# Performance work log

Hardware: AMD Instinct MI355X
Metric: run time of the kernel (lower is better)

The kernel has to match this reference:

```python
import jax, jax.numpy as jnp
import numpy as np

N = 4096
CIN = 128
COUT = 128
J = 2
SLOPE = 0.2        # LeakyReLU negative slope (GAT-style)
NEG = -9.0e15      # mask fill value from the source
ATT = J * COUT     # att_slice


def _leaky(v):
    return jnp.where(v >= 0, v, SLOPE * v)


def setup_inputs() -> dict:
    key = jax.random.key(0)
    ks = jax.random.split(key, 12)
    x = jax.random.normal(ks[0], (N, CIN), dtype=jnp.float32)

    def sparse_op(k):
        kv, km = jax.random.split(k)
        vals = jax.random.normal(kv, (N, N), dtype=jnp.float32)
        mask = jax.random.uniform(km, (N, N)) < 0.05
        return jnp.where(mask, vals, 0.0)

    Lu = sparse_op(ks[1])
    Ld = sparse_op(ks[2])
    P = jax.random.normal(ks[3], (N, N), dtype=jnp.float32) * 0.01  # harmonic projector

    s = 1.0 / np.sqrt(CIN)
    Wi_w = jax.random.uniform(ks[4], (J, CIN, COUT), minval=-s, maxval=s)
    Wi_b = jax.random.uniform(ks[5], (J, COUT), minval=-s, maxval=s)
    Ws_w = jax.random.uniform(ks[6], (J, CIN, COUT), minval=-s, maxval=s)
    Ws_b = jax.random.uniform(ks[7], (J, COUT), minval=-s, maxval=s)
    Wh_w = jax.random.uniform(ks[8], (CIN, COUT), minval=-s, maxval=s)
    Wh_b = jax.random.uniform(ks[9], (COUT,), minval=-s, maxval=s)
    att_irr = jax.random.normal(ks[10], (2 * ATT, 1), dtype=jnp.float32) * 0.1
    att_sol = jax.random.normal(ks[11], (2 * ATT, 1), dtype=jnp.float32) * 0.1
    return {"x": x, "Lu": Lu, "Ld": Ld, "P": P,
            "Wi_w": Wi_w, "Wi_b": Wi_b, "Ws_w": Ws_w, "Ws_b": Ws_b,
            "Wh_w": Wh_w, "Wh_b": Wh_b, "att_irr": att_irr, "att_sol": att_sol}


def reference(x, Lu, Ld, P, Wi_w, Wi_b, Ws_w, Ws_b, Wh_w, Wh_b, att_irr, att_sol):
    n = x.shape[0]
    # concat_j W_irr[j](x) -> [N, J*COUT] (j-major matches torch.cat along dim=1)
    x_irr = (jnp.einsum('nc,jco->njo', x, Wi_w) + Wi_b[None]).reshape(n, ATT)
    x_sol = (jnp.einsum('nc,jco->njo', x, Ws_w) + Ws_b[None]).reshape(n, ATT)

    # GAT-style scores: E[i,j] = leaky(s1[i] + s2[j])
    E_irr = _leaky(x_irr @ att_irr[:ATT] + (x_irr @ att_irr[ATT:]).T)
    E_sol = _leaky(x_sol @ att_sol[:ATT] + (x_sol @ att_sol[ATT:]).T)
    E_irr = jnp.where(Ld != 0, E_irr, NEG)
    E_sol = jnp.where(Lu != 0, E_sol, NEG)
    alpha_irr = jax.nn.softmax(E_irr, axis=1)  # dropout: eval mode -> identity
    alpha_sol = jax.nn.softmax(E_sol, axis=1)

    z = (alpha_irr @ x) @ Wi_w[0] + Wi_b[0] + (alpha_sol @ x) @ Ws_w[0] + Ws_b[0]
    for p in range(1, J):  # Laplacian-power aggregation
        alpha_irr = alpha_irr @ Ld
        alpha_sol = alpha_sol @ Lu
        z = z + (alpha_irr @ x) @ Wi_w[p] + Wi_b[p]
        z = z + (alpha_sol @ x) @ Ws_w[p] + Ws_b[p]
    z = z + (P @ x) @ Wh_w + Wh_b
    return z
```

## Files before the change

kernel.cpp:

```cpp
#include <hip/hip_runtime.h>

#define NN 4096
#define IDX_CAP 512
#define SEG_CAP 160
#define SLOPE 0.2f

typedef float f4_t __attribute__((ext_vector_type(4)));
typedef __bf16 bf8v __attribute__((ext_vector_type(8)));
typedef float f32x16 __attribute__((ext_vector_type(16)));

#define V_OFF     0
#define C_OFF     512
#define BT_OFF    516
#define S_OFF     1024
#define HXI_OFF   32768
#define HXS_OFF   (HXI_OFF + NN*128)
#define UI_OFF    (HXS_OFF + NN*128)
#define US_OFF    (UI_OFF + NN*128)
#define XWH_OFF   (US_OFF + NN*128)
#define OI_OFF    (XWH_OFF + NN*128)
#define OS_OFF    (OI_OFF + NN*128)
#define ZP_OFF    (OS_OFF + NN*128)
#define WS_FLOATS (ZP_OFF + 8*NN*128)
#define IDX_BYTE_OFF ((size_t)WS_FLOATS * 4)
#define CNT_BYTE_OFF (IDX_BYTE_OFF + (size_t)2*NN*IDX_CAP*2)

#define XI(c)   ((c) + (((c) >> 5) << 2))

#define MAP_BR(bid)   (((bid) >> 2) & 1)
#define MAP_ROW(bid)  ((((bid) >> 3) << 2) | ((bid) & 3))

__device__ __forceinline__ unsigned short f2bf(float x) {
  unsigned u = __float_as_uint(x);
  return (unsigned short)((u + 0x7FFFu + ((u >> 16) & 1u)) >> 16);
}
__device__ __forceinline__ float bf2f(unsigned short h) {
  return __uint_as_float(((unsigned)h) << 16);
}
union BFU { unsigned short u[8]; bf8v v; };

__global__ __launch_bounds__(128) void k_prep(
    const float* __restrict__ Wi_w, const float* __restrict__ Wi_b,
    const float* __restrict__ Ws_w, const float* __restrict__ Ws_b,
    const float* __restrict__ Wh_b, const float* __restrict__ att_irr,
    const float* __restrict__ att_sol, float* __restrict__ ws) {
  const int t = threadIdx.x;
  float v1i = 0.f, v2i = 0.f, v1s = 0.f, v2s = 0.f;
  for (int j = 0; j < 2; ++j) {
    for (int o = 0; o < 128; ++o) {
      const float wi = Wi_w[j*16384 + t*128 + o];
      const float wv = Ws_w[j*16384 + t*128 + o];
      v1i += wi * att_irr[j*128 + o];
      v2i += wi * att_irr[256 + j*128 + o];
      v1s += wv * att_sol[j*128 + o];
      v2s += wv * att_sol[256 + j*128 + o];
    }
  }
  ws[V_OFF + t]       = v1i;
  ws[V_OFF + 128 + t] = v2i;
  ws[V_OFF + 256 + t] = v1s;
  ws[V_OFF + 384 + t] = v2s;
  ws[BT_OFF + t] = Wi_b[t] + Wi_b[128 + t] + Ws_b[t] + Ws_b[128 + t] + Wh_b[t];
  if (t < 4) {
    const float* bb = (t < 2) ? Wi_b : Ws_b;
    const float* aa = ((t < 2) ? att_irr : att_sol) + ((t & 1) ? 256 : 0);
    float c = 0.f;
    for (int k = 0; k < 256; ++k) c += bb[k] * aa[k];
    ws[C_OFF + t] = c;
  }
}

__global__ __launch_bounds__(256) void k_pre2(
    const float* __restrict__ x, const float* __restrict__ Wh_w,
    float* __restrict__ ws, unsigned short* __restrict__ xth,
    unsigned short* __restrict__ xtl) {
  __shared__ __align__(16) float At[32][33];
  __shared__ __align__(16) float Wt[32][144];
  const int t = threadIdx.x;

  if (blockIdx.x < 128) {
    const int rb = blockIdx.x;
    const int rg = t >> 4, cg = t & 15;
    const int r0 = rb * 32;
    float acc[2][8];
    #pragma unroll
    for (int i = 0; i < 2; ++i)
      #pragma unroll
      for (int j = 0; j < 8; ++j) acc[i][j] = 0.f;
    for (int k0 = 0; k0 < 128; k0 += 32) {
      __syncthreads();
      {
        const int row = t >> 3, kq = t & 7;
        const float4 av = *(const float4*)&x[(r0 + row)*128 + k0 + kq*4];
        At[row][kq*4+0] = av.x; At[row][kq*4+1] = av.y;
        At[row][kq*4+2] = av.z; At[row][kq*4+3] = av.w;
      }
      #pragma unroll
      for (int l = 0; l < 4; ++l) {
        const int idx = t + l*256;
        const int kr = idx >> 5, c4 = idx & 31;
        const float4 wv = *(const float4*)&Wh_w[(k0 + kr)*128 + c4*4];
        *(float4*)&Wt[kr][XI(c4*4)] = wv;
      }
      __syncthreads();
      #pragma unroll
      for (int k = 0; k < 32; ++k) {
        const float a0 = At[rg*2 + 0][k];
        const float a1 = At[rg*2 + 1][k];
        const float4 b0 = *(const float4*)&Wt[k][XI(cg*8)];
        const float4 b1 = *(const float4*)&Wt[k][XI(cg*8 + 4)];
        acc[0][0] += a0*b0.x; acc[0][1] += a0*b0.y; acc[0][2] += a0*b0.z; acc[0][3] += a0*b0.w;
        acc[0][4] += a0*b1.x; acc[0][5] += a0*b1.y; acc[0][6] += a0*b1.z; acc[0][7] += a0*b1.w;
        acc[1][0] += a1*b0.x; acc[1][1] += a1*b0.y; acc[1][2] += a1*b0.z; acc[1][3] += a1*b0.w;
        acc[1][4] += a1*b1.x; acc[1][5] += a1*b1.y; acc[1][6] += a1*b1.z; acc[1][7] += a1*b1.w;
      }
    }
    #pragma unroll
    for (int i = 0; i < 2; ++i) {
      const int r = r0 + rg*2 + i;
      #pragma unroll
      for (int j = 0; j < 8; ++j) {
        const int c = cg*8 + j;
        const float val = acc[i][j];
        const unsigned short h = f2bf(val);
        const unsigned short l = f2bf(val - bf2f(h));
        xth[(size_t)c*NN + r] = h;
        xtl[(size_t)c*NN + r] = l;
      }
    }
  } else {
    const int wave = t >> 6, lane = t & 63;
    const int row = (blockIdx.x - 128) * 4 + wave;
    const float* v = ws + V_OFF;
    const float x0 = x[row*128 + lane];
    const float x1 = x[row*128 + 64 + lane];
    float p0 = x0 * v[lane]       + x1 * v[64 + lane];
    float p1 = x0 * v[128 + lane] + x1 * v[192 + lane];
    float p2 = x0 * v[256 + lane] + x1 * v[320 + lane];
    float p3 = x0 * v[384 + lane] + x1 * v[448 + lane];
    #pragma unroll
    for (int off = 32; off; off >>= 1) {
      p0 += __shfl_down(p0, off);
      p1 += __shfl_down(p1, off);
      p2 += __shfl_down(p2, off);
      p3 += __shfl_down(p3, off);
    }
    if (lane == 0) {
      ws[S_OFF + row]          = p0 + ws[C_OFF + 0];
      ws[S_OFF + NN + row]     = p1 + ws[C_OFF + 1];
      ws[S_OFF + 2*NN + row]   = p2 + ws[C_OFF + 2];
      ws[S_OFF + 3*NN + row]   = p3 + ws[C_OFF + 3];
    }
  }
}

__global__ __launch_bounds__(256) void k_spmm_emit(
    const float* __restrict__ Ld, const float* __restrict__ Lu,
    const float* __restrict__ x, float* __restrict__ ws,
    unsigned short* __restrict__ idxbuf, int* __restrict__ cntbuf) {
  const int bid = blockIdx.x;
  const int br  = MAP_BR(bid);
  const int row = MAP_ROW(bid);
  const float* __restrict__ Lrow = (br ? Lu : Ld) + (size_t)row * NN;
  float* __restrict__ Hx = ws + (br ? HXS_OFF : HXI_OFF);
  unsigned short* __restrict__ idxg = idxbuf + (size_t)(br*NN + row) * IDX_CAP;
  const int t = threadIdx.x;
  const int w = t >> 6, lane = t & 63;
  const unsigned long long lmask = (1ull << lane) - 1ull;

  __shared__ short jseg[4][SEG_CAP];
  __shared__ float vseg[4][SEG_CAP];
  __shared__ int   wcnt[4];
  __shared__ int   off[5];
  __shared__ short jl[IDX_CAP];
  __shared__ float vl[IDX_CAP];
  __shared__ float red[4][128];

  const f4_t* __restrict__ Lrow4 = (const f4_t*)Lrow;
  f4_t lv[4];
  #pragma unroll
  for (int i = 0; i < 4; ++i) lv[i] = __builtin_nontemporal_load(&Lrow4[i*256 + t]);

  int base = 0;
  #pragma unroll
  for (int i = 0; i < 4; ++i) {
    #pragma unroll
    for (int c = 0; c < 4; ++c) {
      const float v = lv[i][c];
      const unsigned long long bm = __ballot(v != 0.f);
      if (v != 0.f) {
        const int pos = base + (int)__popcll(bm & lmask);
        if (pos < SEG_CAP) {
          jseg[w][pos] = (short)((i*256 + t)*4 + c);
          vseg[w][pos] = v;
        }
      }
      base += (int)__popcll(bm);
    }
  }
  if (lane == 0) wcnt[w] = base;
  __syncthreads();
  if (t == 0) {
    int o = 0, ov = 0;
    #pragma unroll
    for (int s = 0; s < 4; ++s) { off[s] = o; ov |= (wcnt[s] > SEG_CAP); o += wcnt[s]; }
    off[4] = (ov || o > IDX_CAP) ? (IDX_CAP + 1) : o;
    cntbuf[br*NN + row] = off[4];
  }
  __syncthreads();
  const int m = off[4];

  if (m <= IDX_CAP) {
    const int o = off[w], c = wcnt[w];
    for (int k = lane; k < c; k += 64) {
      const short j = jseg[w][k];
      jl[o + k] = j;
      vl[o + k] = vseg[w][k];
      idxg[o + k] = (unsigned short)j;
    }
  }
  __syncthreads();

  if (m <= IDX_CAP) {
    const f4_t* __restrict__ x4 = (const f4_t*)x;
    const int li = lane & 31, half = lane >> 5;
    f4_t acc = {0.f, 0.f, 0.f, 0.f};
    int p = w;
    for (; 2*(p + 12) + 1 < m; p += 16) {
      const int q0 = 2*p + half, q1 = 2*(p+4) + half,
                q2 = 2*(p+8) + half, q3 = 2*(p+12) + half;
      const int j0 = jl[q0], j1 = jl[q1], j2 = jl[q2], j3 = jl[q3];
      const float v0 = vl[q0], v1 = vl[q1], v2 = vl[q2], v3 = vl[q3];
      const f4_t g0 = x4[j0*32 + li];
      const f4_t g1 = x4[j1*32 + li];
      const f4_t g2 = x4[j2*32 + li];
      const f4_t g3 = x4[j3*32 + li];
      acc += v0*g0; acc += v1*g1; acc += v2*g2; acc += v3*g3;
    }
    for (; 2*p < m; p += 4) {
      const int q = 2*p + half;
      if (q < m) acc += vl[q] * x4[jl[q]*32 + li];
    }
    #pragma unroll
    for (int c = 0; c < 4; ++c) acc[c] += __shfl_xor(acc[c], 32);
    if (half == 0) {
      red[w][li*4+0] = acc[0]; red[w][li*4+1] = acc[1];
      red[w][li*4+2] = acc[2]; red[w][li*4+3] = acc[3];
    }
  } else {
    const float2* __restrict__ x2 = (const float2*)x;
    float acc0 = 0.f, acc1 = 0.f;
    for (int j = w*1024; j < (w+1)*1024; ++j) {
      const float v = Lrow[j];
      if (v != 0.f) {
        const float2 g = x2[j*64 + lane];
        acc0 += v*g.x; acc1 += v*g.y;
      }
    }
    red[w][lane*2]     = acc0;
    red[w][lane*2 + 1] = acc1;
  }
  __syncthreads();
  if (t < 128)
    Hx[row*128 + t] = red[0][t] + red[1][t] + red[2][t] + red[3][t];
}

__global__ __launch_bounds__(256) void k_ugemm(
    const float* __restrict__ x, const float* __restrict__ Wi_w,
    const float* __restrict__ Ws_w, float* __restrict__ ws) {
  const int rb = blockIdx.x;
  const int sel = blockIdx.y;
  const float* A[2]; const float* W[2]; float* out;
  if (sel == 0) { A[0]=x; W[0]=Wi_w; A[1]=ws+HXI_OFF; W[1]=Wi_w+16384; out=ws+UI_OFF; }
  else          { A[0]=x; W[0]=Ws_w; A[1]=ws+HXS_OFF; W[1]=Ws_w+16384; out=ws+US_OFF; }

  __shared__ __align__(16) float At[32][33];
  __shared__ __align__(16) float Wt[32][144];
  const int t = threadIdx.x;
  const int rg = t >> 4, cg = t & 15;
  const int r0 = rb * 32;
  float acc[2][8];
  #pragma unroll
  for (int i = 0; i < 2; ++i)
    #pragma unroll
    for (int j = 0; j < 8; ++j) acc[i][j] = 0.f;

  for (int ps = 0; ps < 2; ++ps) {
    const float* __restrict__ Ap = A[ps];
    const float* __restrict__ Wp = W[ps];
    for (int k0 = 0; k0 < 128; k0 += 32) {
      __syncthreads();
      {
        const int row = t >> 3, kq = t & 7;
        const float4 av = *(const float4*)&Ap[(r0 + row)*128 + k0 + kq*4];
        At[row][kq*4+0] = av.x; At[row][kq*4+1] = av.y;
        At[row][kq*4+2] = av.z; At[row][kq*4+3] = av.w;
      }
      #pragma unroll
      for (int l = 0; l < 4; ++l) {
        const int idx = t + l*256;
        const int kr = idx >> 5, c4 = idx & 31;
        const float4 wv = *(const float4*)&Wp[(k0 + kr)*128 + c4*4];
        *(float4*)&Wt[kr][XI(c4*4)] = wv;
      }
      __syncthreads();
      #pragma unroll
      for (int k = 0; k < 32; ++k) {
        const float a0 = At[rg*2 + 0][k];
        const float a1 = At[rg*2 + 1][k];
        const float4 b0 = *(const float4*)&Wt[k][XI(cg*8)];
        const float4 b1 = *(const float4*)&Wt[k][XI(cg*8 + 4)];
        acc[0][0] += a0*b0.x; acc[0][1] += a0*b0.y; acc[0][2] += a0*b0.z; acc[0][3] += a0*b0.w;
        acc[0][4] += a0*b1.x; acc[0][5] += a0*b1.y; acc[0][6] += a0*b1.z; acc[0][7] += a0*b1.w;
        acc[1][0] += a1*b0.x; acc[1][1] += a1*b0.y; acc[1][2] += a1*b0.z; acc[1][3] += a1*b0.w;
        acc[1][4] += a1*b1.x; acc[1][5] += a1*b1.y; acc[1][6] += a1*b1.z; acc[1][7] += a1*b1.w;
      }
    }
  }
  #pragma unroll
  for (int i = 0; i < 2; ++i) {
    const int r = r0 + rg*2 + i;
    #pragma unroll
    for (int j = 0; j < 8; ++j) out[r*128 + cg*8 + j] = acc[i][j];
  }
}

__global__ __launch_bounds__(256) void k_attn(
    const float* __restrict__ Ld, const float* __restrict__ Lu,
    float* __restrict__ ws, const unsigned short* __restrict__ idxbuf,
    const int* __restrict__ cntbuf) {
  const int bid = blockIdx.x;
  const int br  = MAP_BR(bid);
  const int row = MAP_ROW(bid);
  const float* __restrict__ U = ws + (br ? US_OFF : UI_OFF);
  float* __restrict__ O = ws + (br ? OS_OFF : OI_OFF);
  const float s1 = ws[S_OFF + (br ? 2*NN : 0) + row];
  const float* __restrict__ s2a = ws + S_OFF + (br ? 3*NN : NN);
  const int cnt = cntbuf[br*NN + row];
  const int t = threadIdx.x;
  const int w = t >> 6, lane = t & 63;

  __shared__ int   jl[IDX_CAP];
  __shared__ float el[IDX_CAP];
  __shared__ float red[4][128];
  __shared__ float rsum[256];
  __shared__ float dsh[4];

  if (cnt > 0 && cnt <= IDX_CAP) {
    const unsigned short* __restrict__ idx = idxbuf + (size_t)(br*NN + row) * IDX_CAP;
    float dpart = 0.f;
    for (int p = t; p < cnt; p += 256) {
      const int j = idx[p];
      const float sc = s1 + s2a[j];
      const float e = expf(sc >= 0.f ? sc : SLOPE * sc);
      jl[p] = j; el[p] = e; dpart += e;
    }
    rsum[t] = dpart;
    __syncthreads();
    if (t < 128) rsum[t] += rsum[t + 128];
    __syncthreads();
    if (t < 64) {
      float v = rsum[t] + rsum[t + 64];
      #pragma unroll
      for (int off = 32; off; off >>= 1) v += __shfl_down(v, off);
      if (t == 0) dsh[0] = v;
    }
    __syncthreads();
    const float den = dsh[0];
    const f4_t* __restrict__ U4 = (const f4_t*)U;
    const int li = lane & 31, half = lane >> 5;
    f4_t acc = {0.f, 0.f, 0.f, 0.f};
    int p = w;
    for (; 2*(p + 12) + 1 < cnt; p += 16) {
      const int q0 = 2*p + half, q1 = 2*(p+4) + half,
                q2 = 2*(p+8) + half, q3 = 2*(p+12) + half;
      const int j0 = jl[q0], j1 = jl[q1], j2 = jl[q2], j3 = jl[q3];
      const float e0 = el[q0], e1 = el[q1], e2 = el[q2], e3 = el[q3];
      const f4_t g0 = U4[j0*32 + li];
      const f4_t g1 = U4[j1*32 + li];
      const f4_t g2 = U4[j2*32 + li];
      const f4_t g3 = U4[j3*32 + li];
      acc += e0*g0; acc += e1*g1; acc += e2*g2; acc += e3*g3;
    }
    for (; 2*p < cnt; p += 4) {
      const int q = 2*p + half;
      if (q < cnt) acc += el[q] * U4[jl[q]*32 + li];
    }
    #pragma unroll
    for (int c = 0; c < 4; ++c) acc[c] += __shfl_xor(acc[c], 32);
    if (half == 0) {
      red[w][li*4+0] = acc[0]; red[w][li*4+1] = acc[1];
      red[w][li*4+2] = acc[2]; red[w][li*4+3] = acc[3];
    }
    __syncthreads();
    if (t < 128)
      O[row*128 + t] = (red[0][t] + red[1][t] + red[2][t] + red[3][t]) / den;
  } else if (cnt == 0) {
    const float2* __restrict__ U2 = (const float2*)U;
    float acc0 = 0.f, acc1 = 0.f;
    for (int j = w*1024; j < (w+1)*1024; ++j) {
      const float2 g = U2[j*64 + lane];
      acc0 += g.x; acc1 += g.y;
    }
    red[w][lane*2]     = acc0;
    red[w][lane*2 + 1] = acc1;
    __syncthreads();
    if (t < 128)
      O[row*128 + t] = (red[0][t] + red[1][t] + red[2][t] + red[3][t]) * (1.f / NN);
  } else {
    const float* __restrict__ Lrow = (br ? Lu : Ld) + (size_t)row * NN;
    const float2* __restrict__ U2 = (const float2*)U;
    float acc0 = 0.f, acc1 = 0.f, dp = 0.f;
    for (int j = w*1024; j < (w+1)*1024; ++j) {
      const float v = Lrow[j];
      if (v != 0.f) {
        const float sc = s1 + s2a[j];
        const float e = expf(sc >= 0.f ? sc : SLOPE * sc);
        const float2 g = U2[j*64 + lane];
        acc0 += e*g.x; acc1 += e*g.y;
        dp += e;
      }
    }
    if (lane == 0) dsh[w] = dp;
    red[w][lane*2]     = acc0;
    red[w][lane*2 + 1] = acc1;
    __syncthreads();
    const float den = dsh[0] + dsh[1] + dsh[2] + dsh[3];
    if (t < 128)
      O[row*128 + t] = (red[0][t] + red[1][t] + red[2][t] + red[3][t]) / den;
  }
}

__global__ __launch_bounds__(256) void k_pgemm(
    const float* __restrict__ P, const unsigned short* __restrict__ xth,
    const unsigned short* __restrict__ xtl, float* __restrict__ zpart) {
  const int t = threadIdx.x;
  const int w = t >> 6, lane = t & 63;
  const int mt = w & 1, kh = w >> 1;
  const int la = lane & 31;
  const int koff = (lane >> 5) * 8;
  const int r0 = blockIdx.x * 64;
  const int kz = blockIdx.y;
  const int kb = kz * 512 + kh * 256;

  f32x16 acc[4];
  #pragma unroll
  for (int n = 0; n < 4; ++n)
    #pragma unroll
    for (int e = 0; e < 16; ++e) acc[n][e] = 0.f;

  const float* __restrict__ arow = P + (size_t)(r0 + 32*mt + la) * NN + kb + koff;

  for (int s = 0; s < 16; ++s) {
    const int kk = s * 16;
    const float4 a0 = *(const float4*)(arow + kk);
    const float4 a1 = *(const float4*)(arow + kk + 4);
    BFU ah, al;
    #pragma unroll
    for (int i = 0; i < 8; ++i) {
      const float f = (i < 4) ? (&a0.x)[i] : (&a1.x)[i - 4];
      const unsigned short h = f2bf(f);
      ah.u[i] = h;
      al.u[i] = f2bf(f - bf2f(h));
    }
    #pragma unroll
    for (int n = 0; n < 4; ++n) {
      const size_t boff = (size_t)(32*n + la) * NN + kb + kk + koff;
      const bf8v bh = *(const bf8v*)(xth + boff);
      const bf8v bl = *(const bf8v*)(xtl + boff);
      acc[n] = __builtin_amdgcn_mfma_f32_32x32x16_bf16(ah.v, bh, acc[n], 0, 0, 0);
      acc[n] = __builtin_amdgcn_mfma_f32_32x32x16_bf16(al.v, bh, acc[n], 0, 0, 0);
      acc[n] = __builtin_amdgcn_mfma_f32_32x32x16_bf16(ah.v, bl, acc[n], 0, 0, 0);
    }
  }

  __shared__ float red[2][32][128];
  if (kh == 0) {
    #pragma unroll
    for (int n = 0; n < 4; ++n)
      #pragma unroll
      for (int reg = 0; reg < 16; ++reg) {
        const int row = (reg & 3) + 8*(reg >> 2) + 4*(lane >> 5);
        red[mt][row][32*n + la] = acc[n][reg];
      }
  }
  __syncthreads();
  if (kh == 1) {
    float* __restrict__ zp = zpart + (size_t)kz * NN * 128;
    #pragma unroll
    for (int n = 0; n < 4; ++n)
      #pragma unroll
      for (int reg = 0; reg < 16; ++reg) {
        const int row = (reg & 3) + 8*(reg >> 2) + 4*(lane >> 5);
        zp[(size_t)(r0 + 32*mt + row) * 128 + 32*n + la] =
            red[mt][row][32*n + la] + acc[n][reg];
      }
  }
}

__global__ __launch_bounds__(256) void k_combine(const float* __restrict__ ws,
                                                 float* __restrict__ z) {
  const int i = blockIdx.x * 256 + threadIdx.x;
  const int col = i & 127;
  float acc = ws[BT_OFF + col] + ws[OI_OFF + i] + ws[OS_OFF + i];
  #pragma unroll
  for (int kz = 0; kz < 8; ++kz) acc += ws[ZP_OFF + kz*NN*128 + i];
  z[i] = acc;
}

extern "C" void kernel_launch(void* const* d_in, const int* in_sizes, int n_in,
                              void* d_out, int out_size, void* d_ws, size_t ws_size,
                              hipStream_t stream) {
  const float* x       = (const float*)d_in[0];
  const float* Lu      = (const float*)d_in[1];
  const float* Ld      = (const float*)d_in[2];
  const float* P       = (const float*)d_in[3];
  const float* Wi_w    = (const float*)d_in[4];
  const float* Wi_b    = (const float*)d_in[5];
  const float* Ws_w    = (const float*)d_in[6];
  const float* Ws_b    = (const float*)d_in[7];
  const float* Wh_w    = (const float*)d_in[8];
  const float* Wh_b    = (const float*)d_in[9];
  const float* att_irr = (const float*)d_in[10];
  const float* att_sol = (const float*)d_in[11];
  float* z  = (float*)d_out;
  float* ws = (float*)d_ws;
  unsigned short* idxbuf = (unsigned short*)((char*)d_ws + IDX_BYTE_OFF);
  int*            cntbuf = (int*)((char*)d_ws + CNT_BYTE_OFF);
  float*          zpart  = ws + ZP_OFF;
  unsigned short* xth    = (unsigned short*)(ws + XWH_OFF);
  unsigned short* xtl    = xth + (size_t)128 * NN;

  k_prep<<<1, 128, 0, stream>>>(Wi_w, Wi_b, Ws_w, Ws_b, Wh_b, att_irr, att_sol, ws);
  k_pre2<<<1152, 256, 0, stream>>>(x, Wh_w, ws, xth, xtl);
  k_spmm_emit<<<2 * NN, 256, 0, stream>>>(Ld, Lu, x, ws, idxbuf, cntbuf);
  {
    dim3 g(128, 2);
    k_ugemm<<<g, 256, 0, stream>>>(x, Wi_w, Ws_w, ws);
  }
  k_attn<<<2 * NN, 256, 0, stream>>>(Ld, Lu, ws, idxbuf, cntbuf);
  {
    dim3 g(64, 8);
    k_pgemm<<<g, 256, 0, stream>>>(P, xth, xtl, zpart);
  }
  k_combine<<<NN * 128 / 256, 256, 0, stream>>>(ws, z);
}
```

Measured before the change: 362.5 us.

## Store xW_h in MFMA fragment layout and split P-GEMM K across four waves

The bf16 hi/lo copies of x@Wh are now written in a fragment-ordered layout, so each lane reads its B operand as one contiguous 16-byte load instead of scattered strided rows. The P GEMM now uses 32-row tiles with all four waves splitting K, which doubles the grid to 1024 blocks, and P is prefetched one step ahead with nontemporal loads. Partial sums are reduced in two LDS stages before coalesced stores. In exchange, B reuse per block is halved (each block re-reads B for only 32 rows) and there is an extra barrier.

Result: faster. 353.8 us (-2.4%).

```diff
diff --git a/kernel.cpp b/kernel.cpp
--- a/kernel.cpp
+++ b/kernel.cpp
@@ -30,6 +30,9 @@
 #define MAP_BR(bid)   (((bid) >> 2) & 1)
 #define MAP_ROW(bid)  ((((bid) >> 3) << 2) | ((bid) & 3))
 
+#define FRAG(c, k) ((size_t)((k) >> 4) * 2048 + (size_t)((c) >> 5) * 512 \
+                    + (size_t)((((c) & 31) + 32 * (((k) >> 3) & 1)) * 8 + ((k) & 7)))
+
 __device__ __forceinline__ unsigned short f2bf(float x) {
   unsigned u = __float_as_uint(x);
   return (unsigned short)((u + 0x7FFFu + ((u >> 16) & 1u)) >> 16);
@@ -124,8 +127,9 @@
         const float val = acc[i][j];
         const unsigned short h = f2bf(val);
         const unsigned short l = f2bf(val - bf2f(h));
-        xth[(size_t)c*NN + r] = h;
-        xtl[(size_t)c*NN + r] = l;
+        const size_t fa = FRAG(c, r);
+        xth[fa] = h;
+        xtl[fa] = l;
       }
     }
   } else {
@@ -436,12 +440,11 @@
     const unsigned short* __restrict__ xtl, float* __restrict__ zpart) {
   const int t = threadIdx.x;
   const int w = t >> 6, lane = t & 63;
-  const int mt = w & 1, kh = w >> 1;
   const int la = lane & 31;
   const int koff = (lane >> 5) * 8;
-  const int r0 = blockIdx.x * 64;
+  const int r0 = blockIdx.x * 32;
   const int kz = blockIdx.y;
-  const int kb = kz * 512 + kh * 256;
+  const int kb = kz * 512 + w * 128;
 
   f32x16 acc[4];
   #pragma unroll
@@ -449,52 +452,66 @@
     #pragma unroll
     for (int e = 0; e < 16; ++e) acc[n][e] = 0.f;
 
-  const float* __restrict__ arow = P + (size_t)(r0 + 32*mt + la) * NN + kb + koff;
-
-  for (int s = 0; s < 16; ++s) {
-    const int kk = s * 16;
-    const float4 a0 = *(const float4*)(arow + kk);
-    const float4 a1 = *(const float4*)(arow + kk + 4);
+  const float* __restrict__ arow = P + (size_t)(r0 + la) * NN + kb + koff;
+  const unsigned short* __restrict__ bh_base = xth + (size_t)kb * 128 + lane * 8;
+  const unsigned short* __restrict__ bl_base = xtl + (size_t)kb * 128 + lane * 8;
+
+  f4_t a0 = __builtin_nontemporal_load((const f4_t*)arow);
+  f4_t a1 = __builtin_nontemporal_load((const f4_t*)(arow + 4));
+  for (int s = 0; s < 8; ++s) {
+    f4_t na0 = a0, na1 = a1;
+    if (s < 7) {
+      na0 = __builtin_nontemporal_load((const f4_t*)(arow + (s + 1) * 16));
+      na1 = __builtin_nontemporal_load((const f4_t*)(arow + (s + 1) * 16 + 4));
+    }
     BFU ah, al;
     #pragma unroll
     for (int i = 0; i < 8; ++i) {
-      const float f = (i < 4) ? (&a0.x)[i] : (&a1.x)[i - 4];
+      const float f = (i < 4) ? a0[i] : a1[i - 4];
       const unsigned short h = f2bf(f);
       ah.u[i] = h;
       al.u[i] = f2bf(f - bf2f(h));
     }
+    const unsigned short* __restrict__ bh_s = bh_base + s * 2048;
+    const unsigned short* __restrict__ bl_s = bl_base + s * 2048;
     #pragma unroll
     for (int n = 0; n < 4; ++n) {
-      const size_t boff = (size_t)(32*n + la) * NN + kb + kk + koff;
-      const bf8v bh = *(const bf8v*)(xth + boff);
-      const bf8v bl = *(const bf8v*)(xtl + boff);
+      const bf8v bh = *(const bf8v*)(bh_s + n * 512);
+      const bf8v bl = *(const bf8v*)(bl_s + n * 512);
       acc[n] = __builtin_amdgcn_mfma_f32_32x32x16_bf16(ah.v, bh, acc[n], 0, 0, 0);
       acc[n] = __builtin_amdgcn_mfma_f32_32x32x16_bf16(al.v, bh, acc[n], 0, 0, 0);
       acc[n] = __builtin_amdgcn_mfma_f32_32x32x16_bf16(ah.v, bl, acc[n], 0, 0, 0);
     }
+    a0 = na0; a1 = na1;
   }
 
   __shared__ float red[2][32][128];
-  if (kh == 0) {
+  if (w < 2) {
     #pragma unroll
     for (int n = 0; n < 4; ++n)
       #pragma unroll
       for (int reg = 0; reg < 16; ++reg) {
         const int row = (reg & 3) + 8*(reg >> 2) + 4*(lane >> 5);
-        red[mt][row][32*n + la] = acc[n][reg];
+        red[w][row][32*n + la] = acc[n][reg];
       }
   }
   __syncthreads();
-  if (kh == 1) {
-    float* __restrict__ zp = zpart + (size_t)kz * NN * 128;
+  if (w >= 2) {
     #pragma unroll
     for (int n = 0; n < 4; ++n)
       #pragma unroll
       for (int reg = 0; reg < 16; ++reg) {
         const int row = (reg & 3) + 8*(reg >> 2) + 4*(lane >> 5);
-        zp[(size_t)(r0 + 32*mt + row) * 128 + 32*n + la] =
-            red[mt][row][32*n + la] + acc[n][reg];
-      }
+        red[w - 2][row][32*n + la] += acc[n][reg];
+      }
+  }
+  __syncthreads();
+  float* __restrict__ zp = zpart + (size_t)kz * NN * 128;
+  #pragma unroll
+  for (int i = 0; i < 8; ++i) {
+    const int row = w * 8 + i;
+    zp[(size_t)(r0 + row) * 128 + lane]      = red[0][row][lane]      + red[1][row][lane];
+    zp[(size_t)(r0 + row) * 128 + 64 + lane] = red[0][row][64 + lane] + red[1][row][64 + lane];
   }
 }
 
@@ -540,7 +557,7 @@
   }
   k_attn<<<2 * NN, 256, 0, stream>>>(Ld, Lu, ws, idxbuf, cntbuf);
   {
-    dim3 g(64, 8);
+    dim3 g(128, 8);
     k_pgemm<<<g, 256, 0, stream>>>(P, xth, xtl, zpart);
   }
   k_combine<<<NN * 128 / 256, 256, 0, stream>>>(ws, z);
```
